# Kernel optimization log

Measured on AMD Instinct MI355X. Metric: run time of the kernel, lower is better.

## Reference

```python
import jax, jax.numpy as jnp
import numpy as np

BUCKET_BINS = np.array([0, 1, 2, 3, 4, 5, 7, 8, 15, 16, 31, 32, 63, 64])
SPAN_MAX_LEN = 8  # args.span_maximum_length


def _span_indices(L, W):
    """Enumerate all spans of width 1..min(L,W) over a length-L sequence.
    Matches the torch loop: window w contributes starts 0..L-w, end = start+w.
    Returns static numpy arrays (starts, ends, width-bucket ids)."""
    starts, ends = [], []
    for w in range(1, min(L, W) + 1):
        s = np.arange(0, L - w + 1)
        starts.append(s)
        ends.append(s + w)
    starts = np.concatenate(starts)
    ends = np.concatenate(ends)
    widths = ends - starts
    # bucket_embedding: last index ix with width >= bucket_bins[ix]
    buckets = np.searchsorted(BUCKET_BINS, widths, side='right') - 1
    return starts, ends, buckets


def setup_inputs() -> dict:
    key = jax.random.key(0)
    k1, k2 = jax.random.split(key)
    B, L, D, WDIM = 8, 512, 768, 20
    return {
        "x": jax.random.normal(k1, (B, L, D), dtype=jnp.float32),
        "span_width_emb": jax.random.normal(k2, (len(BUCKET_BINS), WDIM), dtype=jnp.float32),
        "batch_max_seq_len": L,
    }


def reference(x, span_width_emb, batch_max_seq_len):
    # x: [B, L, D]; span enumeration is static given (L, W)
    B = x.shape[0]
    starts, ends, buckets = _span_indices(int(batch_max_seq_len), SPAN_MAX_LEN)
    S = starts.shape[0]
    x_start = x[:, starts, :]            # [B, S, D] gather of start tokens
    x_end = x[:, ends - 1, :]            # [B, S, D] gather of end tokens
    w_emb = span_width_emb[buckets]      # [S, WDIM] width-bucket embedding
    w_emb = jnp.broadcast_to(w_emb[None], (B, S, w_emb.shape[-1]))
    # torch.stack(spans, dim=1) with each span = cat(start, end, width_emb)
    return jnp.concatenate([x_start, x_end, w_emb], axis=-1)  # [B, S, 2D+WDIM]
```

## Files before the change

kernel.cpp:

```cpp
#include <hip/hip_runtime.h>


#define B_DIM 8
#define L_DIM 512
#define D_DIM 768
#define W_DIM 20
#define S_TOT 4068
#define ROWF (2 * D_DIM + W_DIM)
#define ROW4 (ROWF / 4)
#define D4 (D_DIM / 4)

__global__ __launch_bounds__(128) void span_rep_kernel(
    const float* __restrict__ x,
    const float* __restrict__ wemb,
    float* __restrict__ out)
{
    const int s = blockIdx.x;
    const int b = blockIdx.y;

    int rem = s;
    int w = 1;
    #pragma unroll 8
    while (rem >= (L_DIM - w + 1)) { rem -= (L_DIM - w + 1); ++w; }
    const int start = rem;
    const int endm1 = start + w - 1;

    const int bucket = (int)((0x765543210ull >> (4 * w)) & 0xF);

    const float4* __restrict__ xs =
        reinterpret_cast<const float4*>(x + ((size_t)b * L_DIM + start) * D_DIM);
    const float4* __restrict__ xe =
        reinterpret_cast<const float4*>(x + ((size_t)b * L_DIM + endm1) * D_DIM);
    const float4* __restrict__ we =
        reinterpret_cast<const float4*>(wemb + (size_t)bucket * W_DIM);
    float4* __restrict__ o =
        reinterpret_cast<float4*>(out + ((size_t)b * S_TOT + s) * (size_t)ROWF);

    for (int j = threadIdx.x; j < ROW4; j += 128) {
        float4 v;
        if (j < D4)            v = xs[j];
        else if (j < 2 * D4)   v = xe[j - D4];
        else                   v = we[j - 2 * D4];
        o[j] = v;
    }
}

extern "C" void kernel_launch(void* const* d_in, const int* in_sizes, int n_in,
                              void* d_out, int out_size, void* d_ws, size_t ws_size,
                              hipStream_t stream) {
    const float* x    = (const float*)d_in[0];
    const float* wemb = (const float*)d_in[1];
    float* out = (float*)d_out;

    dim3 grid(S_TOT, B_DIM);
    span_rep_kernel<<<grid, 128, 0, stream>>>(x, wemb, out);
}
```

Baseline: 216.9 us.

## Flatten span copy into grid-stride float4 loop with nontemporal stores

Replaces the per-span block with a flat grid-stride loop over every float4 of the output. Each thread decodes row, column, span width and start with a division and a comparison ladder. Each thread issues four independent loads before its stores, which writes the output as one uniform stream with more requests in flight. Stores are nontemporal so the large output does not fill the caches. The cost is per-element index arithmetic and scattered gather addresses within a wavefront.

```diff
diff --git a/kernel.cpp b/kernel.cpp
--- a/kernel.cpp
+++ b/kernel.cpp
@@ -1,57 +1,76 @@
 #include <hip/hip_runtime.h>
 
 
-#define B_DIM 8
-#define L_DIM 512
-#define D_DIM 768
-#define W_DIM 20
-#define S_TOT 4068
-#define ROWF (2 * D_DIM + W_DIM)
-#define ROW4 (ROWF / 4)
-#define D4 (D_DIM / 4)
+typedef float f4 __attribute__((ext_vector_type(4)));
 
-__global__ __launch_bounds__(128) void span_rep_kernel(
-    const float* __restrict__ x,
-    const float* __restrict__ wemb,
-    float* __restrict__ out)
+#define D4      192
+#define S_TOT   4068
+#define ROW4    389
+#define TOTAL4  (8 * S_TOT * ROW4)
+
+__device__ __forceinline__ const f4* span_src(
+    int j, const f4* __restrict__ x, const f4* __restrict__ we)
 {
-    const int s = blockIdx.x;
-    const int b = blockIdx.y;
+    unsigned row = (unsigned)j / ROW4;
+    int col = j - (int)row * ROW4;
+    unsigned b = row / S_TOT;
+    int s = (int)row - (int)(b * S_TOT);
 
-    int rem = s;
-    int w = 1;
-    #pragma unroll 8
-    while (rem >= (L_DIM - w + 1)) { rem -= (L_DIM - w + 1); ++w; }
-    const int start = rem;
-    const int endm1 = start + w - 1;
+    int w = 1, cw = 0;
+    if (s >= 512)  { w = 2; cw = 512;  }
+    if (s >= 1023) { w = 3; cw = 1023; }
+    if (s >= 1533) { w = 4; cw = 1533; }
+    if (s >= 2042) { w = 5; cw = 2042; }
+    if (s >= 2550) { w = 6; cw = 2550; }
+    if (s >= 3057) { w = 7; cw = 3057; }
+    if (s >= 3563) { w = 8; cw = 3563; }
+    const int start = s - cw;
 
-    const int bucket = (int)((0x765543210ull >> (4 * w)) & 0xF);
+    if (col < 2 * D4) {
+        int r = (col < D4) ? start : (start + w - 1);
+        int c = (col < D4) ? col : (col - D4);
+        return x + ((b * 512u + (unsigned)r) * (unsigned)D4 + (unsigned)c);
+    } else {
+        int bucket = (int)((0x765543210ull >> (4 * w)) & 0xF);
+        return we + bucket * 5 + (col - 2 * D4);
+    }
+}
 
-    const float4* __restrict__ xs =
-        reinterpret_cast<const float4*>(x + ((size_t)b * L_DIM + start) * D_DIM);
-    const float4* __restrict__ xe =
-        reinterpret_cast<const float4*>(x + ((size_t)b * L_DIM + endm1) * D_DIM);
-    const float4* __restrict__ we =
-        reinterpret_cast<const float4*>(wemb + (size_t)bucket * W_DIM);
-    float4* __restrict__ o =
-        reinterpret_cast<float4*>(out + ((size_t)b * S_TOT + s) * (size_t)ROWF);
+__global__ __launch_bounds__(256) void span_rep_flat(
+    const f4* __restrict__ x,
+    const f4* __restrict__ we,
+    f4* __restrict__ out)
+{
+    const int stride = gridDim.x * 256;
+    int idx = blockIdx.x * 256 + (int)threadIdx.x;
 
-    for (int j = threadIdx.x; j < ROW4; j += 128) {
-        float4 v;
-        if (j < D4)            v = xs[j];
-        else if (j < 2 * D4)   v = xe[j - D4];
-        else                   v = we[j - 2 * D4];
-        o[j] = v;
+    for (; idx < TOTAL4; idx += 4 * stride) {
+        const int j1 = idx + stride;
+        const int j2 = idx + 2 * stride;
+        const int j3 = idx + 3 * stride;
+        const bool p1 = j1 < TOTAL4;
+        const bool p2 = j2 < TOTAL4;
+        const bool p3 = j3 < TOTAL4;
+
+        f4 v0 = *span_src(idx, x, we);
+        f4 v1 = {}, v2 = {}, v3 = {};
+        if (p1) v1 = *span_src(j1, x, we);
+        if (p2) v2 = *span_src(j2, x, we);
+        if (p3) v3 = *span_src(j3, x, we);
+
+        __builtin_nontemporal_store(v0, &out[idx]);
+        if (p1) __builtin_nontemporal_store(v1, &out[j1]);
+        if (p2) __builtin_nontemporal_store(v2, &out[j2]);
+        if (p3) __builtin_nontemporal_store(v3, &out[j3]);
     }
 }
 
 extern "C" void kernel_launch(void* const* d_in, const int* in_sizes, int n_in,
                               void* d_out, int out_size, void* d_ws, size_t ws_size,
                               hipStream_t stream) {
-    const float* x    = (const float*)d_in[0];
-    const float* wemb = (const float*)d_in[1];
-    float* out = (float*)d_out;
+    const f4* x  = (const f4*)d_in[0];
+    const f4* we = (const f4*)d_in[1];
+    f4* out = (f4*)d_out;
 
-    dim3 grid(S_TOT, B_DIM);
-    span_rep_kernel<<<grid, 128, 0, stream>>>(x, wemb, out);
+    span_rep_flat<<<2048, 256, 0, stream>>>(x, we, out);
 }
```

Result: slower. 231.5 us (+6.7%).

## Invert mapping: each block loads one token row and scatters it to all spans

Applied to the files above, without the earlier changes.

Instead of one block per output span gathering its start and end token rows, each block now reads a single input token once and writes it into every span that uses it as start or end, across all 8 widths. Width-embedding tails are written by a separate group of threads. This removes redundant input reads, which were about 16 per token, and launches far fewer blocks. Each block's writes are scattered over many output rows instead of one contiguous row, which may hurt write coalescing.

```diff
diff --git a/kernel.cpp b/kernel.cpp
--- a/kernel.cpp
+++ b/kernel.cpp
@@ -1,57 +1,55 @@
 #include <hip/hip_runtime.h>
 
 
-#define B_DIM 8
+typedef float f4 __attribute__((ext_vector_type(4)));
+
 #define L_DIM 512
-#define D_DIM 768
-#define W_DIM 20
 #define S_TOT 4068
-#define ROWF (2 * D_DIM + W_DIM)
-#define ROW4 (ROWF / 4)
-#define D4 (D_DIM / 4)
+#define ROW4  389
+#define D4    192
 
-__global__ __launch_bounds__(128) void span_rep_kernel(
-    const float* __restrict__ x,
-    const float* __restrict__ wemb,
-    float* __restrict__ out)
+__global__ __launch_bounds__(256) void span_rep_bcast(
+    const f4* __restrict__ x,
+    const f4* __restrict__ we,
+    f4* __restrict__ out)
 {
-    const int s = blockIdx.x;
+    const int r = blockIdx.x;
     const int b = blockIdx.y;
+    const int t = (int)threadIdx.x;
 
-    int rem = s;
-    int w = 1;
-    #pragma unroll 8
-    while (rem >= (L_DIM - w + 1)) { rem -= (L_DIM - w + 1); ++w; }
-    const int start = rem;
-    const int endm1 = start + w - 1;
+    const int cw[8] = {0, 512, 1023, 1533, 2042, 2550, 3057, 3563};
 
-    const int bucket = (int)((0x765543210ull >> (4 * w)) & 0xF);
+    const size_t outB = (size_t)b * S_TOT;
 
-    const float4* __restrict__ xs =
-        reinterpret_cast<const float4*>(x + ((size_t)b * L_DIM + start) * D_DIM);
-    const float4* __restrict__ xe =
-        reinterpret_cast<const float4*>(x + ((size_t)b * L_DIM + endm1) * D_DIM);
-    const float4* __restrict__ we =
-        reinterpret_cast<const float4*>(wemb + (size_t)bucket * W_DIM);
-    float4* __restrict__ o =
-        reinterpret_cast<float4*>(out + ((size_t)b * S_TOT + s) * (size_t)ROWF);
-
-    for (int j = threadIdx.x; j < ROW4; j += 128) {
-        float4 v;
-        if (j < D4)            v = xs[j];
-        else if (j < 2 * D4)   v = xe[j - D4];
-        else                   v = we[j - 2 * D4];
-        o[j] = v;
+    if (t < 192) {
+        const f4 v = x[((size_t)b * L_DIM + r) * D4 + t];
+        #pragma unroll
+        for (int w = 1; w <= 8; ++w) {
+            if (r + w <= L_DIM)
+                out[(outB + cw[w - 1] + r) * ROW4 + t] = v;
+            if (r >= w - 1)
+                out[(outB + cw[w - 1] + r - w + 1) * ROW4 + D4 + t] = v;
+        }
+    } else {
+        const int u = t - 192;
+        if (u < 40) {
+            const int w = u / 5 + 1;
+            const int col = u - (w - 1) * 5;
+            if (r + w <= L_DIM) {
+                const int bucket = (int)((0x765543210ull >> (4 * w)) & 0xF);
+                out[(outB + cw[w - 1] + r) * ROW4 + 2 * D4 + col] = we[bucket * 5 + col];
+            }
+        }
     }
 }
 
 extern "C" void kernel_launch(void* const* d_in, const int* in_sizes, int n_in,
                               void* d_out, int out_size, void* d_ws, size_t ws_size,
                               hipStream_t stream) {
-    const float* x    = (const float*)d_in[0];
-    const float* wemb = (const float*)d_in[1];
-    float* out = (float*)d_out;
+    const f4* x  = (const f4*)d_in[0];
+    const f4* we = (const f4*)d_in[1];
+    f4* out = (f4*)d_out;
 
-    dim3 grid(S_TOT, B_DIM);
-    span_rep_kernel<<<grid, 128, 0, stream>>>(x, wemb, out);
+    dim3 grid(L_DIM, 8);
+    span_rep_bcast<<<grid, 256, 0, stream>>>(x, we, out);
 }
```

After: 209.6 us. 1.03x faster.
